# Kernel optimization log

Hardware: AMD Instinct MI355X
Metric: run time of the kernel (lower is better)

## Reference

```python
import jax, jax.numpy as jnp
import numpy as np

DT = 0.2   # dt
T = 30     # free-phase relaxation steps


def rho(x):
    return jnp.clip(x, 0.0, 1.0)


def rhop(x):
    return ((x >= 0.0) & (x <= 1.0)).astype(x.dtype)


def setup_inputs() -> dict:
    key = jax.random.key(0)
    ks = jax.random.split(key, 10)
    B = 2048
    L = [1024, 2048, 2048, 2048]  # fcLayers
    s0 = jax.random.uniform(ks[0], (B, L[0]), dtype=jnp.float32)
    s1 = jax.random.uniform(ks[1], (B, L[1]), dtype=jnp.float32)
    s2 = jax.random.uniform(ks[2], (B, L[2]), dtype=jnp.float32)
    data = jax.random.uniform(ks[3], (B, L[3]), dtype=jnp.float32)
    # W[i] = Linear(fcLayers[i+1], fcLayers[i]) -> weight [L[i], L[i+1]], fan_in = L[i+1]
    W0 = jax.random.normal(ks[4], (L[0], L[1]), dtype=jnp.float32) / np.float32(np.sqrt(L[1]))
    b0 = jax.random.normal(ks[5], (L[0],), dtype=jnp.float32) * np.float32(0.01)
    W1 = jax.random.normal(ks[6], (L[1], L[2]), dtype=jnp.float32) / np.float32(np.sqrt(L[2]))
    b1 = jax.random.normal(ks[7], (L[1],), dtype=jnp.float32) * np.float32(0.01)
    W2 = jax.random.normal(ks[8], (L[2], L[3]), dtype=jnp.float32) / np.float32(np.sqrt(L[3]))
    b2 = jax.random.normal(ks[9], (L[2],), dtype=jnp.float32) * np.float32(0.01)
    return {"s0": s0, "s1": s1, "s2": s2, "data": data,
            "W0": W0, "b0": b0, "W1": W1, "b1": b1, "W2": W2, "b2": b2}


def reference(s0, s1, s2, data, W0, b0, W1, b1, W2, b2):
    # Free-phase (beta=None, target=None, loss='MSE') -> stepper_c iterated T times.
    # s = [s0, s1, s2, data]; data (last element) is never updated.
    rd = rho(data)  # fixed input drive, precomputed once

    def step(carry, _):
        s0, s1, s2 = carry
        r0, r1, r2 = rho(s0), rho(s1), rho(s2)
        # dsdt[0] = -s0 + rhop(s0) * W0(rho(s1))
        d0 = -s0 + rhop(s0) * (r1 @ W0.T + b0)
        # dsdt[1] = -s1 + rhop(s1) * ( W1(rho(s2)) + rho(s0) @ W0 )
        d1 = -s1 + rhop(s1) * (r2 @ W1.T + b1 + r0 @ W0)
        # dsdt[2] = -s2 + rhop(s2) * ( W2(rho(data)) + rho(s1) @ W1 )
        d2 = -s2 + rhop(s2) * (rd @ W2.T + b2 + r1 @ W1)
        n0 = jnp.clip(s0 + DT * d0, 0.0, 1.0)
        n1 = jnp.clip(s1 + DT * d1, 0.0, 1.0)
        n2 = jnp.clip(s2 + DT * d2, 0.0, 1.0)
        return (n0, n1, n2), None

    (f0, f1, f2), _ = jax.lax.scan(step, (s0, s1, s2), None, length=T)
    return (f0, f1, f2)
```

## Files before the change

### kernel.cpp

```cpp
#include <hip/hip_runtime.h>
#include <stdint.h>

#define BM 128
#define BN 128
#define BK 64

typedef __bf16 bf16x8 __attribute__((ext_vector_type(8)));
typedef float f32x4 __attribute__((ext_vector_type(4)));

__device__ __forceinline__ float bf2f(uint16_t u) {
  union { uint32_t u32; float f; } x; x.u32 = ((uint32_t)u) << 16; return x.f;
}
__device__ __forceinline__ uint16_t f2bf(float f) {
  uint32_t x = __float_as_uint(f);
  uint32_t r = (x + 0x7FFFu + ((x >> 16) & 1u)) >> 16;
  return (uint16_t)r;
}

__device__ __forceinline__ void gload_lds16(const uint16_t* g, uint16_t* l) {
  __builtin_amdgcn_global_load_lds(
      (const __attribute__((address_space(1))) uint32_t*)g,
      (__attribute__((address_space(3))) uint32_t*)l, 16, 0, 0);
}

__device__ __forceinline__ void gemm_tile(
    const uint16_t* __restrict__ A, int ldA,
    const uint16_t* __restrict__ Bt, int ldB,
    int m0, int n0, int K,
    uint16_t* ldsA, uint16_t* ldsB, f32x4 acc[4][4])
{
  const int t  = threadIdx.x;
  const int ln = t & 63;
  const int wv = t >> 6;
  const int wr = wv >> 1, wc = wv & 1;

  const int row = t >> 3;
  const int gc  = (t & 7) ^ (row & 7);
  const uint16_t* ga = A  + (size_t)(m0 + row) * ldA + (gc << 3);
  const uint16_t* gb = Bt + (size_t)(n0 + row) * ldB + (gc << 3);
  uint16_t* la = ldsA + (t << 3);
  uint16_t* lb = ldsB + (t << 3);

  for (int kt = 0; kt < K; kt += BK) {
    __syncthreads();
#pragma unroll
    for (int c = 0; c < 4; ++c) {
      gload_lds16(ga + (size_t)(c * 32) * ldA, la + c * 2048);
      gload_lds16(gb + (size_t)(c * 32) * ldB, lb + c * 2048);
    }
    ga += BK; gb += BK;
    __syncthreads();

#pragma unroll
    for (int kk = 0; kk < 2; ++kk) {
      const int kc = (kk << 2) + (ln >> 4);
      const int sw = (kc ^ (ln & 7)) << 3;
      bf16x8 af[4], bfr[4];
#pragma unroll
      for (int mt = 0; mt < 4; ++mt)
        af[mt] = *(const bf16x8*)&ldsA[((wr << 6) + (mt << 4) + (ln & 15)) * BK + sw];
#pragma unroll
      for (int nt = 0; nt < 4; ++nt)
        bfr[nt] = *(const bf16x8*)&ldsB[((wc << 6) + (nt << 4) + (ln & 15)) * BK + sw];
#pragma unroll
      for (int mt = 0; mt < 4; ++mt)
#pragma unroll
        for (int nt = 0; nt < 4; ++nt)
          acc[mt][nt] = __builtin_amdgcn_mfma_f32_16x16x32_bf16(
              af[mt], bfr[nt], acc[mt][nt], 0, 0, 0);
    }
  }
}

__global__ void step_kernel(
    const uint16_t* __restrict__ s0b_c, const uint16_t* __restrict__ s1b_c,
    const uint16_t* __restrict__ s2b_c,
    uint16_t* __restrict__ s0b_n, uint16_t* __restrict__ s1b_n,
    uint16_t* __restrict__ s2b_n,
    const uint16_t* __restrict__ W0b, const uint16_t* __restrict__ W0Tb,
    const uint16_t* __restrict__ W1b, const uint16_t* __restrict__ W1Tb,
    const float* __restrict__ b0, const float* __restrict__ b1,
    const float* __restrict__ c2f,
    float* __restrict__ s0f, float* __restrict__ s1f, float* __restrict__ s2f)
{
  __shared__ uint16_t ldsA[BM * BK];
  __shared__ uint16_t ldsB[BN * BK];

  f32x4 acc[4][4];
  const f32x4 z = {0.f, 0.f, 0.f, 0.f};
#pragma unroll
  for (int i = 0; i < 4; ++i)
#pragma unroll
    for (int j = 0; j < 4; ++j) acc[i][j] = z;

  const int x = blockIdx.x & 7;
  const int j = blockIdx.x >> 3;
  int mode, bm, bn;
  if (j < 16) {
    mode = 0; bm = (x << 1) + (j >> 3); bn = j & 7;
    gemm_tile(s1b_c, 2048, W0b, 2048, bm * BM, bn * BN, 2048, ldsA, ldsB, acc);
  } else if (j < 48) {
    mode = 1; const int u = j - 16; bm = (x << 1) + (u >> 4); bn = u & 15;
    gemm_tile(s2b_c, 2048, W1b, 2048, bm * BM, bn * BN, 2048, ldsA, ldsB, acc);
    gemm_tile(s0b_c, 1024, W0Tb, 1024, bm * BM, bn * BN, 1024, ldsA, ldsB, acc);
  } else {
    mode = 2; const int u = j - 48; bm = (x << 1) + (u >> 4); bn = u & 15;
    gemm_tile(s1b_c, 2048, W1Tb, 2048, bm * BM, bn * BN, 2048, ldsA, ldsB, acc);
  }

  const int t = threadIdx.x, wv = t >> 6, ln = t & 63;
  const int wr = wv >> 1, wc = wv & 1;
  const int rb = (ln >> 4) << 2, cc = ln & 15;
  const int m0 = bm * BM, n0 = bn * BN;

#pragma unroll
  for (int mt = 0; mt < 4; ++mt) {
#pragma unroll
    for (int nt = 0; nt < 4; ++nt) {
      const int gn = n0 + (wc << 6) + (nt << 4) + cc;
      float add = 0.f;
      if (mode == 0) add = b0[gn];
      else if (mode == 1) add = b1[gn];
#pragma unroll
      for (int r = 0; r < 4; ++r) {
        const int gm = m0 + (wr << 6) + (mt << 4) + rb + r;
        const float pre = acc[mt][nt][r];
        if (mode == 0) {
          const size_t ix = (size_t)gm * 1024 + gn;
          float nv = 0.8f * s0f[ix] + 0.2f * (pre + add);
          nv = fminf(fmaxf(nv, 0.f), 1.f);
          s0f[ix] = nv;
          s0b_n[ix] = f2bf(nv);
        } else if (mode == 1) {
          const size_t ix = (size_t)gm * 2048 + gn;
          float nv = 0.8f * s1f[ix] + 0.2f * (pre + add);
          nv = fminf(fmaxf(nv, 0.f), 1.f);
          s1f[ix] = nv;
          s1b_n[ix] = f2bf(nv);
        } else {
          const size_t ix = (size_t)gm * 2048 + gn;
          float nv = 0.8f * s2f[ix] + 0.2f * (pre + c2f[ix]);
          nv = fminf(fmaxf(nv, 0.f), 1.f);
          s2f[ix] = nv;
          s2b_n[ix] = f2bf(nv);
        }
      }
    }
  }
}

__global__ void c2_kernel(const uint16_t* __restrict__ datab,
                          const uint16_t* __restrict__ W2b,
                          const float* __restrict__ b2,
                          float* __restrict__ c2f)
{
  __shared__ uint16_t ldsA[BM * BK];
  __shared__ uint16_t ldsB[BN * BK];
  f32x4 acc[4][4];
  const f32x4 z = {0.f, 0.f, 0.f, 0.f};
#pragma unroll
  for (int i = 0; i < 4; ++i)
#pragma unroll
    for (int j = 0; j < 4; ++j) acc[i][j] = z;

  const int bm = blockIdx.x >> 4, bn = blockIdx.x & 15;
  gemm_tile(datab, 2048, W2b, 2048, bm * BM, bn * BN, 2048, ldsA, ldsB, acc);

  const int t = threadIdx.x, wv = t >> 6, ln = t & 63;
  const int wr = wv >> 1, wc = wv & 1;
  const int rb = (ln >> 4) << 2, cc = ln & 15;
  const int m0 = bm * BM, n0 = bn * BN;
#pragma unroll
  for (int mt = 0; mt < 4; ++mt)
#pragma unroll
    for (int nt = 0; nt < 4; ++nt) {
      const int gn = n0 + (wc << 6) + (nt << 4) + cc;
      const float bb = b2[gn];
#pragma unroll
      for (int r = 0; r < 4; ++r) {
        const int gm = m0 + (wr << 6) + (mt << 4) + rb + r;
        c2f[(size_t)gm * 2048 + gn] = acc[mt][nt][r] + bb;
      }
    }
}

__global__ void conv_k(const float* __restrict__ src, uint16_t* __restrict__ dst)
{
  const size_t i4 = ((size_t)blockIdx.x * 256 + threadIdx.x) << 2;
  const float4 v = *(const float4*)(src + i4);
  ushort4 o;
  o.x = f2bf(v.x); o.y = f2bf(v.y); o.z = f2bf(v.z); o.w = f2bf(v.w);
  *(ushort4*)(dst + i4) = o;
}

__global__ void convT_k(const float* __restrict__ src, uint16_t* __restrict__ dst,
                        int ldS, int ldD)
{
  __shared__ uint16_t tile[32][33];
  const int r0 = blockIdx.y * 32, c0 = blockIdx.x * 32;
  tile[threadIdx.y][threadIdx.x] =
      f2bf(src[(size_t)(r0 + threadIdx.y) * ldS + c0 + threadIdx.x]);
  __syncthreads();
  dst[(size_t)(c0 + threadIdx.y) * ldD + r0 + threadIdx.x] = tile[threadIdx.x][threadIdx.y];
}

__global__ void init_state(const float* __restrict__ in,
                           float* __restrict__ sf, uint16_t* __restrict__ sb)
{
  const size_t i4 = ((size_t)blockIdx.x * 256 + threadIdx.x) << 2;
  const float4 v = *(const float4*)(in + i4);
  *(float4*)(sf + i4) = v;
  ushort4 o;
  o.x = f2bf(v.x); o.y = f2bf(v.y); o.z = f2bf(v.z); o.w = f2bf(v.w);
  *(ushort4*)(sb + i4) = o;
}

extern "C" void kernel_launch(void* const* d_in, const int* in_sizes, int n_in,
                              void* d_out, int out_size, void* d_ws, size_t ws_size,
                              hipStream_t stream) {
  const float* s0   = (const float*)d_in[0];
  const float* s1   = (const float*)d_in[1];
  const float* s2   = (const float*)d_in[2];
  const float* data = (const float*)d_in[3];
  const float* W0   = (const float*)d_in[4];
  const float* b0   = (const float*)d_in[5];
  const float* W1   = (const float*)d_in[6];
  const float* b1   = (const float*)d_in[7];
  const float* W2   = (const float*)d_in[8];
  const float* b2   = (const float*)d_in[9];

  float* s0f = (float*)d_out;
  float* s1f = s0f + 2048ull * 1024;
  float* s2f = s1f + 2048ull * 2048;

  char* ws = (char*)d_ws;
  size_t off = 0;
  auto alloc = [&](size_t bytes) -> char* {
    char* p = ws + off; off += (bytes + 255) & ~(size_t)255; return p;
  };
  uint16_t* W0b    = (uint16_t*)alloc(1024ull * 2048 * 2);
  uint16_t* W0Tb   = (uint16_t*)alloc(2048ull * 1024 * 2);
  uint16_t* W1b    = (uint16_t*)alloc(2048ull * 2048 * 2);
  uint16_t* W1Tb   = (uint16_t*)alloc(2048ull * 2048 * 2);
  float*    c2f    = (float*)   alloc(2048ull * 2048 * 4);
  uint16_t* s0b[2] = { (uint16_t*)alloc(2048ull * 1024 * 2),
                       (uint16_t*)alloc(2048ull * 1024 * 2) };
  uint16_t* s1b[2] = { (uint16_t*)alloc(2048ull * 2048 * 2),
                       (uint16_t*)alloc(2048ull * 2048 * 2) };
  uint16_t* s2b[2] = { (uint16_t*)alloc(2048ull * 2048 * 2),
                       (uint16_t*)alloc(2048ull * 2048 * 2) };
  (void)ws_size; (void)in_sizes; (void)n_in; (void)out_size;

  conv_k<<<1024 * 2048 / 1024, 256, 0, stream>>>(W0, W0b);
  conv_k<<<2048 * 2048 / 1024, 256, 0, stream>>>(W1, W1b);
  dim3 tb(32, 32);
  convT_k<<<dim3(64, 32), tb, 0, stream>>>(W0, W0Tb, 2048, 1024);
  convT_k<<<dim3(64, 64), tb, 0, stream>>>(W1, W1Tb, 2048, 2048);
  conv_k<<<2048 * 2048 / 1024, 256, 0, stream>>>(data, s1b[1]);
  conv_k<<<2048 * 2048 / 1024, 256, 0, stream>>>(W2, s2b[1]);
  c2_kernel<<<256, 256, 0, stream>>>(s1b[1], s2b[1], b2, c2f);

  init_state<<<2048 * 1024 / 1024, 256, 0, stream>>>(s0, s0f, s0b[0]);
  init_state<<<2048 * 2048 / 1024, 256, 0, stream>>>(s1, s1f, s1b[0]);
  init_state<<<2048 * 2048 / 1024, 256, 0, stream>>>(s2, s2f, s2b[0]);

  for (int it = 0; it < 30; ++it) {
    const int c = it & 1, n = c ^ 1;
    step_kernel<<<640, 256, 0, stream>>>(
        s0b[c], s1b[c], s2b[c], s0b[n], s1b[n], s2b[n],
        W0b, W0Tb, W1b, W1Tb, b0, b1, c2f, s0f, s1f, s2f);
  }
}
```

Before: 2.442 ms.

## Double-buffer LDS tiles in GEMM loop and reorder block scheduling by cost

The GEMM tile loop now uses two LDS buffers: the next K-slice is issued via global_load_lds before computing on the current one, with one barrier per iteration instead of two. Block-to-work mapping is reordered so the heavier mode-1 tiles (two GEMMs) are dispatched first, followed by mode-2 and then mode-0 tiles. The LDS footprint doubles to 64KB per block, which may reduce occupancy. Correctness depends on the async LDS loads being complete before the barrier, since no explicit vmcnt wait is added.

```diff
diff --git a/kernel.cpp b/kernel.cpp
--- a/kernel.cpp
+++ b/kernel.cpp
@@ -4,6 +4,7 @@
 #define BM 128
 #define BN 128
 #define BK 64
+#define BUFE 8192
 
 typedef __bf16 bf16x8 __attribute__((ext_vector_type(8)));
 typedef float f32x4 __attribute__((ext_vector_type(4)));
@@ -41,16 +42,28 @@
   uint16_t* la = ldsA + (t << 3);
   uint16_t* lb = ldsB + (t << 3);
 
-  for (int kt = 0; kt < K; kt += BK) {
-    __syncthreads();
-#pragma unroll
-    for (int c = 0; c < 4; ++c) {
-      gload_lds16(ga + (size_t)(c * 32) * ldA, la + c * 2048);
-      gload_lds16(gb + (size_t)(c * 32) * ldB, lb + c * 2048);
-    }
-    ga += BK; gb += BK;
-    __syncthreads();
-
+  const int nIter = K >> 6;
+
+#pragma unroll
+  for (int c = 0; c < 4; ++c) {
+    gload_lds16(ga + (size_t)(c * 32) * ldA, la + c * 2048);
+    gload_lds16(gb + (size_t)(c * 32) * ldB, lb + c * 2048);
+  }
+  ga += BK; gb += BK;
+  __syncthreads();
+
+  for (int kt = 0; kt < nIter; ++kt) {
+    const int cur = kt & 1;
+    if (kt + 1 < nIter) {
+      const int no = (cur ^ 1) * BUFE;
+#pragma unroll
+      for (int c = 0; c < 4; ++c) {
+        gload_lds16(ga + (size_t)(c * 32) * ldA, la + no + c * 2048);
+        gload_lds16(gb + (size_t)(c * 32) * ldB, lb + no + c * 2048);
+      }
+      ga += BK; gb += BK;
+    }
+    const int co = cur * BUFE;
 #pragma unroll
     for (int kk = 0; kk < 2; ++kk) {
       const int kc = (kk << 2) + (ln >> 4);
@@ -58,10 +71,10 @@
       bf16x8 af[4], bfr[4];
 #pragma unroll
       for (int mt = 0; mt < 4; ++mt)
-        af[mt] = *(const bf16x8*)&ldsA[((wr << 6) + (mt << 4) + (ln & 15)) * BK + sw];
+        af[mt] = *(const bf16x8*)&ldsA[co + ((wr << 6) + (mt << 4) + (ln & 15)) * BK + sw];
 #pragma unroll
       for (int nt = 0; nt < 4; ++nt)
-        bfr[nt] = *(const bf16x8*)&ldsB[((wc << 6) + (nt << 4) + (ln & 15)) * BK + sw];
+        bfr[nt] = *(const bf16x8*)&ldsB[co + ((wc << 6) + (nt << 4) + (ln & 15)) * BK + sw];
 #pragma unroll
       for (int mt = 0; mt < 4; ++mt)
 #pragma unroll
@@ -69,6 +82,7 @@
           acc[mt][nt] = __builtin_amdgcn_mfma_f32_16x16x32_bf16(
               af[mt], bfr[nt], acc[mt][nt], 0, 0, 0);
     }
+    __syncthreads();
   }
 }
 
@@ -83,8 +97,8 @@
     const float* __restrict__ c2f,
     float* __restrict__ s0f, float* __restrict__ s1f, float* __restrict__ s2f)
 {
-  __shared__ uint16_t ldsA[BM * BK];
-  __shared__ uint16_t ldsB[BN * BK];
+  __shared__ uint16_t ldsA[2 * BUFE];
+  __shared__ uint16_t ldsB[2 * BUFE];
 
   f32x4 acc[4][4];
   const f32x4 z = {0.f, 0.f, 0.f, 0.f};
@@ -93,19 +107,21 @@
 #pragma unroll
     for (int j = 0; j < 4; ++j) acc[i][j] = z;
 
-  const int x = blockIdx.x & 7;
-  const int j = blockIdx.x >> 3;
+  const int b = blockIdx.x;
   int mode, bm, bn;
-  if (j < 16) {
-    mode = 0; bm = (x << 1) + (j >> 3); bn = j & 7;
-    gemm_tile(s1b_c, 2048, W0b, 2048, bm * BM, bn * BN, 2048, ldsA, ldsB, acc);
-  } else if (j < 48) {
-    mode = 1; const int u = j - 16; bm = (x << 1) + (u >> 4); bn = u & 15;
+  if (b < 256) {
+    mode = 1; const int x = b & 7, j = b >> 3;
+    bm = (x << 1) + (j >> 4); bn = j & 15;
     gemm_tile(s2b_c, 2048, W1b, 2048, bm * BM, bn * BN, 2048, ldsA, ldsB, acc);
     gemm_tile(s0b_c, 1024, W0Tb, 1024, bm * BM, bn * BN, 1024, ldsA, ldsB, acc);
+  } else if (b < 512) {
+    mode = 2; const int u = b - 256, x = u & 7, j = u >> 3;
+    bm = (x << 1) + (j >> 4); bn = j & 15;
+    gemm_tile(s1b_c, 2048, W1Tb, 2048, bm * BM, bn * BN, 2048, ldsA, ldsB, acc);
   } else {
-    mode = 2; const int u = j - 48; bm = (x << 1) + (u >> 4); bn = u & 15;
-    gemm_tile(s1b_c, 2048, W1Tb, 2048, bm * BM, bn * BN, 2048, ldsA, ldsB, acc);
+    mode = 0; const int u = b - 512, x = u & 7, j = u >> 3;
+    bm = (x << 1) + (j >> 3); bn = j & 7;
+    gemm_tile(s1b_c, 2048, W0b, 2048, bm * BM, bn * BN, 2048, ldsA, ldsB, acc);
   }
 
   const int t = threadIdx.x, wv = t >> 6, ln = t & 63;
@@ -154,8 +170,8 @@
                           const float* __restrict__ b2,
                           float* __restrict__ c2f)
 {
-  __shared__ uint16_t ldsA[BM * BK];
-  __shared__ uint16_t ldsB[BN * BK];
+  __shared__ uint16_t ldsA[2 * BUFE];
+  __shared__ uint16_t ldsB[2 * BUFE];
   f32x4 acc[4][4];
   const f32x4 z = {0.f, 0.f, 0.f, 0.f};
 #pragma unroll
```

New measurement: 3.908 ms. 60.0% more time.
